# Kernel optimization log

Measured on AMD Instinct MI355X. Metric: run time of the kernel, lower is better.

## Reference

```python
import jax, jax.numpy as jnp
import numpy as np

B, N, E = 8, 2048, 2048  # requires N == E (see bmm(value, attn^T) constraint)

def setup_inputs() -> dict:
    key = jax.random.key(0)
    k1, k2, k3 = jax.random.split(key, 3)
    inputs = jax.random.normal(k1, (B, N, E), dtype=jnp.float32)
    # nn.Linear(embed_size, embed_size): weight [E,E], bias [E]
    W = jax.random.normal(k2, (E, E), dtype=jnp.float32) * (1.0 / np.sqrt(E))
    b = jax.random.normal(k3, (E,), dtype=jnp.float32) * 0.01
    gamma = jnp.zeros((), dtype=jnp.float32)  # nn.Parameter(torch.tensor(0.0))
    return {"inputs": inputs, "W": W, "b": b, "gamma": gamma}

def reference(inputs, W, b, gamma):
    # query = Linear(inputs); key = value = inputs
    query = jnp.einsum('bne,fe->bnf', inputs, W) + b          # [B,N,E]
    # scores = bmm(query, key^T) + gamma  -> [B,N,N]
    scores = jnp.einsum('bne,bme->bnm', query, inputs) + gamma
    # softmax over dim=1 (rows, NOT the usual last dim)
    attn = jax.nn.softmax(scores, axis=1)                      # [B,N,N]
    # output = bmm(value, attn^T): out[b,n,m] = sum_e value[b,n,e]*attn[b,m,e]
    out = jnp.einsum('bne,bme->bnm', inputs, attn)             # [B,N,N]
    return out
```

## Files before the change

kernel.cpp:

```cpp
#include <hip/hip_runtime.h>
#include <stdint.h>


typedef _Float16 f16;
typedef f16 f16x8 __attribute__((ext_vector_type(8)));
typedef f16 f16x4 __attribute__((ext_vector_type(4)));
typedef float f32x4 __attribute__((ext_vector_type(4)));

#define ND 2048
#define NNL 4194304L
#define NT 32

static __device__ __forceinline__ void stage16(const void* g, void* l) {
  __builtin_amdgcn_global_load_lds(
      (const __attribute__((address_space(1))) uint32_t*)g,
      (__attribute__((address_space(3))) uint32_t*)l, 16, 0, 0);
}

__global__ void cvt_f16(const float* __restrict__ x, f16* __restrict__ h, int n4) {
  int i = blockIdx.x * 256 + threadIdx.x;
  if (i >= n4) return;
  float4 v = reinterpret_cast<const float4*>(x)[i];
  f16x4 o;
  o.x = (f16)v.x; o.y = (f16)v.y; o.z = (f16)v.z; o.w = (f16)v.w;
  reinterpret_cast<f16x4*>(h)[i] = o;
}

#define RB(d_, o_, kh_) ((((d_) << 2) | ((o_) << 1) | (kh_)) * 16384)

#define STG(gp_, ro_, t_, kh_)                                           \
  do {                                                                   \
    stage16((gp_) + (long)(t_) * 128 + (kh_) * 64, smem + (ro_) + ld0);  \
    stage16((gp_) + 524288L + (long)(t_) * 128 + (kh_) * 64,             \
            smem + (ro_) + ld1);                                         \
  } while (0)

#define FENCE asm volatile("" ::: "memory")

#define SYNC(vm_)                                                        \
  do {                                                                   \
    asm volatile("s_waitcnt vmcnt(" #vm_ ") lgkmcnt(0)" ::: "memory");   \
    __builtin_amdgcn_s_barrier();                                        \
    FENCE;                                                               \
  } while (0)

#define PHASE(d_, mh_, kh_, RDB_, STAGE_)                                     \
  do {                                                                        \
    const char* ra_ = smem + RB(d_, 0, kh_) + (mh_) * 4096 + aoff;            \
    f16x8 af[4];                                                              \
    af[0] = *(const f16x8*)(ra_);                                             \
    af[1] = *(const f16x8*)(ra_ + 1024);                                      \
    af[2] = *(const f16x8*)(ra_ + 2048);                                      \
    af[3] = *(const f16x8*)(ra_ + 3072);                                      \
    if (RDB_) {                                                               \
      const char* rb_ = smem + RB(d_, 1, kh_) + boff;                         \
      bf[0] = *(const f16x8*)(rb_);                                           \
      bf[1] = *(const f16x8*)(rb_ + 1024);                                    \
      bf[2] = *(const f16x8*)(rb_ + 2048);                                    \
      bf[3] = *(const f16x8*)(rb_ + 3072);                                    \
    }                                                                         \
    STAGE_                                                                    \
    __builtin_amdgcn_s_setprio(1);                                            \
    _Pragma("unroll") for (int mt_ = 0; mt_ < 4; ++mt_) {                     \
      _Pragma("unroll") for (int nt_ = 0; nt_ < 4; ++nt_) {                   \
        acc[(mh_) * 4 + mt_][nt_] = __builtin_amdgcn_mfma_f32_16x16x32_f16(   \
            af[mt_], bf[nt_], acc[(mh_) * 4 + mt_][nt_], 0, 0, 0);            \
      }                                                                       \
    }                                                                         \
    __builtin_amdgcn_s_setprio(0);                                            \
  } while (0)

template <int MODE>
__launch_bounds__(512, 2) __global__
void gemm256(const f16* __restrict__ A, long sA, const f16* __restrict__ B, long sB,
             const float* __restrict__ bias, const float* __restrict__ gamma,
             float* __restrict__ Cf, f16* __restrict__ Ch,
             float* __restrict__ Mp, float* __restrict__ Sp) {
  __shared__ char smem[131072];

  const int bz = blockIdx.z;
  const long tm = (long)blockIdx.y * 256;
  const long tn = (long)blockIdx.x * 256;
  const int tid = threadIdx.x;
  const int lane = tid & 63;
  const int wid = tid >> 6;
  const int wm = (wid >> 2) << 7;
  const int wn = (wid & 3) << 6;

  const int sg = (tid & 3) ^ ((tid >> 3) & 3);
  const char* gA = (const char*)(A + bz * sA + tm * ND) + (long)(tid >> 2) * 4096 + sg * 16;
  const char* gB = (const char*)(B + bz * sB + tn * ND) + (long)(tid >> 2) * 4096 + sg * 16;
  const uint32_t ld0 = tid * 16u;
  const uint32_t ld1 = 8192u + tid * 16u;

  const int segsw = (((lane >> 4) ^ ((lane >> 1) & 3)) << 4);
  const int lrow = lane & 15;
  const int aoff = (wm + lrow) * 64 + segsw;
  const int boff = (wn + lrow) * 64 + segsw;

  f32x4 acc[8][4] = {};
  f16x8 bf[4];

  STG(gA, RB(0, 0, 0), 0, 0);
  STG(gB, RB(0, 1, 0), 0, 0);
  STG(gA, RB(0, 0, 1), 0, 1);
  STG(gB, RB(0, 1, 1), 0, 1);
  STG(gA, RB(1, 0, 0), 1, 0);
  STG(gB, RB(1, 1, 0), 1, 0);
  asm volatile("s_waitcnt vmcnt(8)" ::: "memory");
  __builtin_amdgcn_s_barrier();
  FENCE;

#pragma unroll 2
  for (int t = 0; t < NT - 2; ++t) {
    const int d = t & 1;
    const int e = d ^ 1;
    PHASE(d, 0, 0, 1, STG(gA, RB(e, 0, 1), t + 1, 1););
    PHASE(d, 1, 0, 0, STG(gB, RB(e, 1, 1), t + 1, 1););
    SYNC(8);
    PHASE(d, 0, 1, 1, STG(gA, RB(d, 0, 0), t + 2, 0););
    PHASE(d, 1, 1, 0, STG(gB, RB(d, 1, 0), t + 2, 0););
    SYNC(8);
  }
  {
    PHASE(0, 0, 0, 1, STG(gA, RB(1, 0, 1), NT - 1, 1););
    PHASE(0, 1, 0, 0, STG(gB, RB(1, 1, 1), NT - 1, 1););
    SYNC(8);
    PHASE(0, 0, 1, 1, ;);
    PHASE(0, 1, 1, 0, ;);
    SYNC(4);
  }
  {
    PHASE(1, 0, 0, 1, ;);
    PHASE(1, 1, 0, 0, ;);
    SYNC(0);
    PHASE(1, 0, 1, 1, ;);
    PHASE(1, 1, 1, 0, ;);
  }

  const int rr = (lane >> 4) << 2;
  const int cc = lane & 15;
  const long cb = (long)bz * NNL;
  if constexpr (MODE == 1) {
#pragma unroll
    for (int nt = 0; nt < 4; ++nt) {
      const long col = tn + wn + nt * 16 + cc;
      const float bj = bias[col];
#pragma unroll
      for (int mt = 0; mt < 8; ++mt) {
#pragma unroll
        for (int r = 0; r < 4; ++r) {
          const long row = tm + wm + mt * 16 + rr + r;
          Ch[cb + row * ND + col] = (f16)(acc[mt][nt][r] + bj);
        }
      }
    }
  } else if constexpr (MODE == 0) {
    const float g = gamma ? gamma[0] : 0.0f;
#pragma unroll
    for (int mt = 0; mt < 8; ++mt) {
#pragma unroll
      for (int nt = 0; nt < 4; ++nt) {
#pragma unroll
        for (int r = 0; r < 4; ++r) {
          const long row = tm + wm + mt * 16 + rr + r;
          const long col = tn + wn + nt * 16 + cc;
          Cf[cb + row * ND + col] = acc[mt][nt][r] + g;
        }
      }
    }
  } else {
    const float g = gamma[0];
    __syncthreads();
    float* redm = (float*)smem;
    float* reds = redm + 512;
#pragma unroll
    for (int nt = 0; nt < 4; ++nt) {
      float ml = -3.4e38f;
#pragma unroll
      for (int mt = 0; mt < 8; ++mt)
#pragma unroll
        for (int r = 0; r < 4; ++r)
          ml = fmaxf(ml, acc[mt][nt][r] + g);
      float sl = 0.f;
#pragma unroll
      for (int mt = 0; mt < 8; ++mt)
#pragma unroll
        for (int r = 0; r < 4; ++r)
          sl += __expf(acc[mt][nt][r] + g - ml);
#pragma unroll
      for (int off = 16; off < 64; off <<= 1) {
        float pm = __shfl_xor(ml, off, 64);
        float ps = __shfl_xor(sl, off, 64);
        float nm = fmaxf(ml, pm);
        sl = sl * __expf(ml - nm) + ps * __expf(pm - nm);
        ml = nm;
      }
      if ((lane >> 4) == 0) {
        redm[wid * 64 + nt * 16 + lrow] = ml;
        reds[wid * 64 + nt * 16 + lrow] = sl;
      }
    }
    __syncthreads();
    if (tid < 256) {
      const float mA = redm[tid], sA = reds[tid];
      const float mB = redm[256 + tid], sB = reds[256 + tid];
      const float m = fmaxf(mA, mB);
      const float s = sA * __expf(mA - m) + sB * __expf(mB - m);
      const long o = ((long)bz * 8 + blockIdx.y) * ND + tn + tid;
      Mp[o] = m;
      Sp[o] = s;
    }
#pragma unroll
    for (int mt = 0; mt < 8; ++mt) {
#pragma unroll
      for (int nt = 0; nt < 4; ++nt) {
#pragma unroll
        for (int r = 0; r < 4; ++r) {
          const long row = tm + wm + mt * 16 + rr + r;
          const long col = tn + wn + nt * 16 + cc;
          Cf[cb + row * ND + col] = acc[mt][nt][r] + g;
        }
      }
    }
  }
}

__global__ void stats_combine(const float* __restrict__ Mp, const float* __restrict__ Sp,
                              float* __restrict__ Mx, float* __restrict__ Rs) {
  const int col = blockIdx.x * 256 + threadIdx.x;
  const int b = blockIdx.y;
  float m = -3.4e38f, s = 0.f;
  for (int k = 0; k < 8; ++k) {
    const long o = ((long)b * 8 + k) * ND + col;
    float mk = Mp[o], sk = Sp[o];
    float nm = fmaxf(m, mk);
    s = s * __expf(m - nm) + sk * __expf(mk - nm);
    m = nm;
  }
  Mx[(long)b * ND + col] = m;
  Rs[(long)b * ND + col] = 1.0f / s;
}

__global__ void scale_exp_kernel(const float* __restrict__ S, const float* __restrict__ Mx,
                                 const float* __restrict__ Rs, f16* __restrict__ A) {
  const long i4 = (long)blockIdx.x * 256 + threadIdx.x;
  const long i = i4 * 4;
  const int b = (int)(i >> 22);
  const int col = (int)(i & 2047);
  float4 s = reinterpret_cast<const float4*>(S)[i4];
  float4 m4 = *reinterpret_cast<const float4*>(&Mx[(long)b * ND + col]);
  float4 r4 = *reinterpret_cast<const float4*>(&Rs[(long)b * ND + col]);
  f16x4 o;
  o.x = (f16)(__expf(s.x - m4.x) * r4.x);
  o.y = (f16)(__expf(s.y - m4.y) * r4.y);
  o.z = (f16)(__expf(s.z - m4.z) * r4.z);
  o.w = (f16)(__expf(s.w - m4.w) * r4.w);
  reinterpret_cast<f16x4*>(A)[i4] = o;
}

extern "C" void kernel_launch(void* const* d_in, const int* in_sizes, int n_in,
                              void* d_out, int out_size, void* d_ws, size_t ws_size,
                              hipStream_t stream) {
  (void)in_sizes; (void)n_in; (void)out_size;
  const float* X = (const float*)d_in[0];
  const float* W = (const float*)d_in[1];
  const float* bias = (const float*)d_in[2];
  const float* gamma = (const float*)d_in[3];

  char* ws = (char*)d_ws;
  f16* Xh = (f16*)(ws);
  f16* Wh = (f16*)(ws + 67108864L);
  f16* Qh = (f16*)(ws + 75497472L);
  float* S = (float*)(ws + 142606336L);
  float* Mp = (float*)(ws + 276824064L);
  float* Sp = (float*)(ws + 277348352L);
  float* Mx = (float*)(ws + 277872640L);
  float* Rs = (float*)(ws + 277938176L);
  f16* Amat = Qh;
  if (ws_size < 278003712UL) return;

  cvt_f16<<<32768, 256, 0, stream>>>(X, Xh, 8388608);
  cvt_f16<<<4096, 256, 0, stream>>>(W, Wh, 1048576);

  dim3 gg(8, 8, 8), bb(512);
  gemm256<1><<<gg, bb, 0, stream>>>(Xh, NNL, Wh, 0L, bias, nullptr, nullptr, Qh,
                                    nullptr, nullptr);
  gemm256<2><<<gg, bb, 0, stream>>>(Qh, NNL, Xh, NNL, nullptr, gamma, S, nullptr,
                                    Mp, Sp);
  stats_combine<<<dim3(8, 8), 256, 0, stream>>>(Mp, Sp, Mx, Rs);
  scale_exp_kernel<<<32768, 256, 0, stream>>>(S, Mx, Rs, Amat);
  gemm256<0><<<gg, bb, 0, stream>>>(Xh, NNL, Amat, NNL, nullptr, nullptr,
                                    (float*)d_out, nullptr, nullptr, nullptr);
}
```

Measured before the change: 672.8 us.

## Store scores as fp16, remap tile order, and widen scale-exp kernel vectors

The scores GEMM now writes the intermediate score matrix in fp16 instead of fp32. Before computing the column softmax statistics it rounds the accumulators to fp16, so the statistics match the values stored. The scale/exp kernel reads and writes 8 fp16 values per thread, halving the traffic of this memory-bound pass. Block indices are also remapped to a swizzled tile order to change L2 locality. Storing scores in fp16 loses precision before the exp, and the mode-0 gamma add is dropped.

```diff
diff --git a/kernel.cpp b/kernel.cpp
--- a/kernel.cpp
+++ b/kernel.cpp
@@ -79,8 +79,10 @@
   __shared__ char smem[131072];
 
   const int bz = blockIdx.z;
-  const long tm = (long)blockIdx.y * 256;
-  const long tn = (long)blockIdx.x * 256;
+  const int bx = ((blockIdx.x & 1) << 2) | (blockIdx.y & 3);
+  const int by = (((blockIdx.x >> 1) & 3) << 1) | (blockIdx.y >> 2);
+  const long tm = (long)by * 256;
+  const long tn = (long)bx * 256;
   const int tid = threadIdx.x;
   const int lane = tid & 63;
   const int wid = tid >> 6;
@@ -156,7 +158,6 @@
       }
     }
   } else if constexpr (MODE == 0) {
-    const float g = gamma ? gamma[0] : 0.0f;
 #pragma unroll
     for (int mt = 0; mt < 8; ++mt) {
 #pragma unroll
@@ -165,12 +166,19 @@
         for (int r = 0; r < 4; ++r) {
           const long row = tm + wm + mt * 16 + rr + r;
           const long col = tn + wn + nt * 16 + cc;
-          Cf[cb + row * ND + col] = acc[mt][nt][r] + g;
+          Cf[cb + row * ND + col] = acc[mt][nt][r];
         }
       }
     }
   } else {
     const float g = gamma[0];
+#pragma unroll
+    for (int mt = 0; mt < 8; ++mt)
+#pragma unroll
+      for (int nt = 0; nt < 4; ++nt)
+#pragma unroll
+        for (int r = 0; r < 4; ++r)
+          acc[mt][nt][r] = (float)(f16)(acc[mt][nt][r] + g);
     __syncthreads();
     float* redm = (float*)smem;
     float* reds = redm + 512;
@@ -181,13 +189,13 @@
       for (int mt = 0; mt < 8; ++mt)
 #pragma unroll
         for (int r = 0; r < 4; ++r)
-          ml = fmaxf(ml, acc[mt][nt][r] + g);
+          ml = fmaxf(ml, acc[mt][nt][r]);
       float sl = 0.f;
 #pragma unroll
       for (int mt = 0; mt < 8; ++mt)
 #pragma unroll
         for (int r = 0; r < 4; ++r)
-          sl += __expf(acc[mt][nt][r] + g - ml);
+          sl += __expf(acc[mt][nt][r] - ml);
 #pragma unroll
       for (int off = 16; off < 64; off <<= 1) {
         float pm = __shfl_xor(ml, off, 64);
@@ -207,7 +215,7 @@
       const float mB = redm[256 + tid], sB = reds[256 + tid];
       const float m = fmaxf(mA, mB);
       const float s = sA * __expf(mA - m) + sB * __expf(mB - m);
-      const long o = ((long)bz * 8 + blockIdx.y) * ND + tn + tid;
+      const long o = ((long)bz * 8 + by) * ND + tn + tid;
       Mp[o] = m;
       Sp[o] = s;
     }
@@ -219,7 +227,7 @@
         for (int r = 0; r < 4; ++r) {
           const long row = tm + wm + mt * 16 + rr + r;
           const long col = tn + wn + nt * 16 + cc;
-          Cf[cb + row * ND + col] = acc[mt][nt][r] + g;
+          Ch[cb + row * ND + col] = (f16)acc[mt][nt][r];
         }
       }
     }
@@ -242,21 +250,29 @@
   Rs[(long)b * ND + col] = 1.0f / s;
 }
 
-__global__ void scale_exp_kernel(const float* __restrict__ S, const float* __restrict__ Mx,
+__global__ void scale_exp_kernel(const f16* __restrict__ S, const float* __restrict__ Mx,
                                  const float* __restrict__ Rs, f16* __restrict__ A) {
-  const long i4 = (long)blockIdx.x * 256 + threadIdx.x;
-  const long i = i4 * 4;
+  const long i8 = (long)blockIdx.x * 256 + threadIdx.x;
+  const long i = i8 * 8;
   const int b = (int)(i >> 22);
   const int col = (int)(i & 2047);
-  float4 s = reinterpret_cast<const float4*>(S)[i4];
-  float4 m4 = *reinterpret_cast<const float4*>(&Mx[(long)b * ND + col]);
-  float4 r4 = *reinterpret_cast<const float4*>(&Rs[(long)b * ND + col]);
-  f16x4 o;
-  o.x = (f16)(__expf(s.x - m4.x) * r4.x);
-  o.y = (f16)(__expf(s.y - m4.y) * r4.y);
-  o.z = (f16)(__expf(s.z - m4.z) * r4.z);
-  o.w = (f16)(__expf(s.w - m4.w) * r4.w);
-  reinterpret_cast<f16x4*>(A)[i4] = o;
+  f16x8 s = reinterpret_cast<const f16x8*>(S)[i8];
+  const float* mp = &Mx[(long)b * ND + col];
+  const float* rp = &Rs[(long)b * ND + col];
+  float4 m0 = *reinterpret_cast<const float4*>(mp);
+  float4 m1 = *reinterpret_cast<const float4*>(mp + 4);
+  float4 r0 = *reinterpret_cast<const float4*>(rp);
+  float4 r1 = *reinterpret_cast<const float4*>(rp + 4);
+  f16x8 o;
+  o[0] = (f16)(__expf((float)s[0] - m0.x) * r0.x);
+  o[1] = (f16)(__expf((float)s[1] - m0.y) * r0.y);
+  o[2] = (f16)(__expf((float)s[2] - m0.z) * r0.z);
+  o[3] = (f16)(__expf((float)s[3] - m0.w) * r0.w);
+  o[4] = (f16)(__expf((float)s[4] - m1.x) * r1.x);
+  o[5] = (f16)(__expf((float)s[5] - m1.y) * r1.y);
+  o[6] = (f16)(__expf((float)s[6] - m1.z) * r1.z);
+  o[7] = (f16)(__expf((float)s[7] - m1.w) * r1.w);
+  reinterpret_cast<f16x8*>(A)[i8] = o;
 }
 
 extern "C" void kernel_launch(void* const* d_in, const int* in_sizes, int n_in,
@@ -272,7 +288,7 @@
   f16* Xh = (f16*)(ws);
   f16* Wh = (f16*)(ws + 67108864L);
   f16* Qh = (f16*)(ws + 75497472L);
-  float* S = (float*)(ws + 142606336L);
+  f16* Sh = (f16*)(ws + 142606336L);
   float* Mp = (float*)(ws + 276824064L);
   float* Sp = (float*)(ws + 277348352L);
   float* Mx = (float*)(ws + 277872640L);
@@ -286,10 +302,10 @@
   dim3 gg(8, 8, 8), bb(512);
   gemm256<1><<<gg, bb, 0, stream>>>(Xh, NNL, Wh, 0L, bias, nullptr, nullptr, Qh,
                                     nullptr, nullptr);
-  gemm256<2><<<gg, bb, 0, stream>>>(Qh, NNL, Xh, NNL, nullptr, gamma, S, nullptr,
+  gemm256<2><<<gg, bb, 0, stream>>>(Qh, NNL, Xh, NNL, nullptr, gamma, nullptr, Sh,
                                     Mp, Sp);
   stats_combine<<<dim3(8, 8), 256, 0, stream>>>(Mp, Sp, Mx, Rs);
-  scale_exp_kernel<<<32768, 256, 0, stream>>>(S, Mx, Rs, Amat);
+  scale_exp_kernel<<<16384, 256, 0, stream>>>(Sh, Mx, Rs, Amat);
   gemm256<0><<<gg, bb, 0, stream>>>(Xh, NNL, Amat, NNL, nullptr, nullptr,
                                     (float*)d_out, nullptr, nullptr, nullptr);
 }
```

Result: faster. 627.6 us (-6.7%).
